# Optimization experiments

Hardware: AMD Instinct MI355X
Metric: run time of the kernel (lower is better)

## Reference

```python
import jax, jax.numpy as jnp
import numpy as np

N, IN_F, E, EDGE_F, H, C = 50000, 128, 800000, 32, 4, 32
NEG_SLOPE = 0.2
EPS = 1e-16


def setup_inputs() -> dict:
    key = jax.random.key(0)
    ks = jax.random.split(key, 10)
    s = lambda *sh: 1.0 / np.sqrt(sh[-1])
    return {
        "node_features": jax.random.normal(ks[0], (N, IN_F), jnp.float32),
        "edge_features": jax.random.normal(ks[1], (E, EDGE_F), jnp.float32),
        "edge_index": jax.random.randint(ks[2], (2, E), 0, N, jnp.int32),
        # GATConv params
        "W_gat": jax.random.normal(ks[3], (H * C, IN_F), jnp.float32) * s(IN_F),
        "att_src": jax.random.normal(ks[4], (H, C), jnp.float32) * s(C),
        "att_dst": jax.random.normal(ks[5], (H, C), jnp.float32) * s(C),
        "att_edge": jax.random.normal(ks[6], (H, C), jnp.float32) * s(C),
        "bias": jnp.zeros((H * C,), jnp.float32),
        # edge_linear and skip_connection weights
        "W_edge": jax.random.normal(ks[7], (H * C, EDGE_F), jnp.float32) * s(EDGE_F),
        "W_skip": jax.random.normal(ks[8], (H * C, IN_F), jnp.float32) * s(IN_F),
    }


def reference(node_features, edge_features, edge_index, W_gat, att_src, att_dst,
              att_edge, bias, W_edge, W_skip):
    src, dst = edge_index[0], edge_index[1]
    # edge_linear + view(-1, H, C)
    e_attr = (edge_features @ W_edge.T).reshape(E, H, C)
    # GATConv: per-head linear transform of nodes -> [N, H, C]
    x = (node_features @ W_gat.T).reshape(N, H, C)
    # attention logits: a_src.x_i + a_dst.x_j + a_edge.e  -> [E, H]
    a_src = jnp.einsum('nhc,hc->nh', x, att_src)
    a_dst = jnp.einsum('nhc,hc->nh', x, att_dst)
    a_edge = jnp.einsum('ehc,hc->eh', e_attr, att_edge)
    alpha = jax.nn.leaky_relu(a_src[src] + a_dst[dst] + a_edge, NEG_SLOPE)
    # segment softmax over incoming edges of each destination node
    m = jax.ops.segment_max(alpha, dst, num_segments=N)  # [N, H]
    m = jnp.where(jnp.isfinite(m), m, 0.0)
    ex = jnp.exp(alpha - m[dst])
    denom = jax.ops.segment_sum(ex, dst, num_segments=N)  # [N, H]
    attn = ex / (denom[dst] + EPS)  # [E, H]
    # message = alpha * x_src ; scatter-add to destination
    msg = x[src] * attn[:, :, None]  # [E, H, C]
    out = jax.ops.segment_sum(msg, dst, num_segments=N)  # [N, H, C]
    out = out.reshape(N, H * C) + bias  # concat=True
    # skip connection + ELU activation
    out = out + node_features @ W_skip.T
    return jax.nn.elu(out)
```

## Files before the change

kernel.cpp:

```cpp
#include <hip/hip_runtime.h>
#include <hip/hip_bf16.h>

constexpr int N_NODES = 50000;
constexpr int IN_F    = 128;
constexpr long E_EDGES = 800000;
constexpr int EDGE_F  = 32;
constexpr int H_HEADS = 4;
constexpr int C_CH    = 32;
constexpr int HC      = 128;
constexpr float NEG_SLOPE = 0.2f;
constexpr float EPS = 1e-16f;
constexpr int B_HIST = 64;
constexpr int B_WCAT = 8;
constexpr int CHUNK  = (int)(E_EDGES / B_HIST);
constexpr int HW8    = N_NODES / 4;
constexpr int NB_SCAN = (N_NODES + 255) / 256;
constexpr int NB_A    = (N_NODES + 3) / 4;
constexpr int NB_EL4  = (int)((E_EDGES + 1023) / 1024);
constexpr int NB_AE10 = (int)((E_EDGES + 511) / 512);
constexpr float SM_SHIFT = 12.0f;

typedef __attribute__((ext_vector_type(8))) short bf16x8;
typedef __attribute__((ext_vector_type(4))) float f32x4;

__device__ __forceinline__ unsigned short f2b(float f) {
    __hip_bfloat16 h = __float2bfloat16(f);
    return *reinterpret_cast<unsigned short*>(&h);
}
__device__ __forceinline__ float b2f_lo(unsigned v) { return __uint_as_float(v << 16); }
__device__ __forceinline__ float b2f_hi(unsigned v) { return __uint_as_float(v & 0xffff0000u); }

__global__ __launch_bounds__(1024) void mega1_kernel(
    const int* __restrict__ dst, unsigned int* __restrict__ histB,
    unsigned short* __restrict__ rank16, const float* __restrict__ ef,
    const float* __restrict__ We, const float* __restrict__ att_edge,
    const float* __restrict__ Wg, const float* __restrict__ Ws,
    unsigned short* __restrict__ wcat, float* __restrict__ ae)
{
    __shared__ unsigned int h[HW8];
    __shared__ float wf_lds[128];
    const int b = blockIdx.x, t = threadIdx.x;

    if (b < B_HIST) {
        for (int i = t; i < HW8; i += 1024) h[i] = 0;
        __syncthreads();
        const int e0 = b * CHUNK;
        for (int i = t; i < CHUNK; i += 1024) {
            int d = dst[e0 + i];
            int sh = (d & 3) * 8;
            unsigned old = atomicAdd(&h[d >> 2], 1u << sh);
            rank16[e0 + i] = (unsigned short)((old >> sh) & 0xFFu);
        }
        __syncthreads();
        unsigned int* outp = histB + (size_t)b * HW8;
        for (int i = t; i < HW8; i += 1024) outp[i] = h[i];
        return;
    }

    if (b < B_HIST + B_WCAT) {
        int i = ((b - B_HIST) * 1024 + t) * 4;
        const float* srcp = (i < 16384) ? (Wg + i) : (Ws + i - 16384);
        float4 v = *(const float4*)srcp;
        ushort4 o;
        o.x = f2b(v.x); o.y = f2b(v.y); o.z = f2b(v.z); o.w = f2b(v.w);
        *(ushort4*)&wcat[i] = o;
        return;
    }

    if (t < 128) {
        int hh = t >> 5, f = t & 31;
        float acc = 0.f;
#pragma unroll
        for (int c = 0; c < C_CH; ++c)
            acc = fmaf(We[(hh * C_CH + c) * EDGE_F + f], att_edge[hh * C_CH + c], acc);
        wf_lds[t] = acc;
    }
    __syncthreads();

    const int l = t & 63, wv = t >> 6;
    const int sub = l & 3, eIdx = l >> 2;
    const long eb = (long)(b - B_HIST - B_WCAT) * 512 + wv * 32 + eIdx;
    const float4* ef4 = (const float4*)ef;
    float4 wa[4], wb[4];
#pragma unroll
    for (int hh = 0; hh < 4; ++hh) {
        wa[hh] = *(const float4*)&wf_lds[hh * 32 + sub * 4];
        wb[hh] = *(const float4*)&wf_lds[hh * 32 + 16 + sub * 4];
    }

    if (eb < E_EDGES) {
        float4 a0 = ef4[eb * 8 + sub];
        float4 b0 = ef4[eb * 8 + 4 + sub];
        float p[4];
#pragma unroll
        for (int hh = 0; hh < 4; ++hh) {
            float acc = 0.f;
            acc = fmaf(a0.x, wa[hh].x, acc); acc = fmaf(a0.y, wa[hh].y, acc);
            acc = fmaf(a0.z, wa[hh].z, acc); acc = fmaf(a0.w, wa[hh].w, acc);
            acc = fmaf(b0.x, wb[hh].x, acc); acc = fmaf(b0.y, wb[hh].y, acc);
            acc = fmaf(b0.z, wb[hh].z, acc); acc = fmaf(b0.w, wb[hh].w, acc);
            p[hh] = acc;
        }
#pragma unroll
        for (int hh = 0; hh < 4; ++hh) {
            p[hh] += __shfl_xor(p[hh], 1);
            p[hh] += __shfl_xor(p[hh], 2);
        }
        float v0 = (sub == 0) ? p[0] : (sub == 1) ? p[1] : (sub == 2) ? p[2] : p[3];
        ae[eb * 4 + sub] = v0;
    }
    if (eb + 16 < E_EDGES) {
        float4 a1 = ef4[(eb + 16) * 8 + sub];
        float4 b1 = ef4[(eb + 16) * 8 + 4 + sub];
        float p[4];
#pragma unroll
        for (int hh = 0; hh < 4; ++hh) {
            float acc = 0.f;
            acc = fmaf(a1.x, wa[hh].x, acc); acc = fmaf(a1.y, wa[hh].y, acc);
            acc = fmaf(a1.z, wa[hh].z, acc); acc = fmaf(a1.w, wa[hh].w, acc);
            acc = fmaf(b1.x, wb[hh].x, acc); acc = fmaf(b1.y, wb[hh].y, acc);
            acc = fmaf(b1.z, wb[hh].z, acc); acc = fmaf(b1.w, wb[hh].w, acc);
            p[hh] = acc;
        }
#pragma unroll
        for (int hh = 0; hh < 4; ++hh) {
            p[hh] += __shfl_xor(p[hh], 1);
            p[hh] += __shfl_xor(p[hh], 2);
        }
        float v1 = (sub == 0) ? p[0] : (sub == 1) ? p[1] : (sub == 2) ? p[2] : p[3];
        ae[(eb + 16) * 4 + sub] = v1;
    }
}

__global__ __launch_bounds__(256) void mfma_gemm_kernel(
    const float* __restrict__ nf, const unsigned short* __restrict__ wcat,
    const float* __restrict__ bias, unsigned short* __restrict__ xb,
    float* __restrict__ out)
{
    const int t  = threadIdx.x;
    const int w  = t >> 6;
    const int l  = t & 63;
    const int lr = l & 15;
    const int lk = l >> 4;
    const int n0 = blockIdx.x * 64;

    bf16x8 bfr[4][4];
#pragma unroll
    for (int nfr = 0; nfr < 4; ++nfr)
#pragma unroll
        for (int ks = 0; ks < 4; ++ks)
            bfr[nfr][ks] = *(const bf16x8*)&wcat[(w * 64 + nfr * 16 + lr) * 128 + ks * 32 + lk * 8];

    f32x4 acc[4][4];
#pragma unroll
    for (int mf = 0; mf < 4; ++mf)
#pragma unroll
        for (int nfr = 0; nfr < 4; ++nfr)
            acc[mf][nfr] = (f32x4){0.f, 0.f, 0.f, 0.f};

#pragma unroll
    for (int ks = 0; ks < 4; ++ks) {
        bf16x8 afr[4];
#pragma unroll
        for (int mf = 0; mf < 4; ++mf) {
            int row = n0 + mf * 16 + lr;
            row = row < N_NODES ? row : N_NODES - 1;
            const float* ap = nf + (size_t)row * IN_F + ks * 32 + lk * 8;
            float4 a0 = *(const float4*)ap;
            float4 a1 = *(const float4*)(ap + 4);
            bf16x8 f;
            f[0] = (short)f2b(a0.x); f[1] = (short)f2b(a0.y);
            f[2] = (short)f2b(a0.z); f[3] = (short)f2b(a0.w);
            f[4] = (short)f2b(a1.x); f[5] = (short)f2b(a1.y);
            f[6] = (short)f2b(a1.z); f[7] = (short)f2b(a1.w);
            afr[mf] = f;
        }
#pragma unroll
        for (int mf = 0; mf < 4; ++mf)
#pragma unroll
            for (int nfr = 0; nfr < 4; ++nfr)
                acc[mf][nfr] = __builtin_amdgcn_mfma_f32_16x16x32_bf16(
                    afr[mf], bfr[nfr][ks], acc[mf][nfr], 0, 0, 0);
    }

#pragma unroll
    for (int nfr = 0; nfr < 4; ++nfr) {
        const int gc = w * 64 + nfr * 16 + lr;
        if (gc < HC) {
#pragma unroll
            for (int mf = 0; mf < 4; ++mf)
#pragma unroll
                for (int r = 0; r < 4; ++r) {
                    int m = n0 + mf * 16 + lk * 4 + r;
                    if (m < N_NODES) xb[(size_t)m * HC + gc] = f2b(acc[mf][nfr][r]);
                }
        } else {
            const float bv = bias[gc - HC];
#pragma unroll
            for (int mf = 0; mf < 4; ++mf)
#pragma unroll
                for (int r = 0; r < 4; ++r) {
                    int m = n0 + mf * 16 + lk * 4 + r;
                    if (m < N_NODES) out[(size_t)m * HC + gc - HC] = acc[mf][nfr][r] + bv;
                }
        }
    }
}

__global__ __launch_bounds__(256) void scan1_a_kernel(
    const unsigned int* __restrict__ histB, int* __restrict__ row_ptr,
    int* __restrict__ blocksum, const unsigned int* __restrict__ xb32,
    const float* __restrict__ att_src, const float* __restrict__ att_dst,
    float* __restrict__ asrc, float* __restrict__ adst)
{
    const int b = blockIdx.x, t = threadIdx.x;
    if (b < NB_SCAN) {
        __shared__ int s[256];
        int i = b * 256 + t;
        int v = 0;
        if (i < N_NODES) {
            int w = i >> 2, sh = (i & 3) * 8;
#pragma unroll 8
            for (int bb = 0; bb < B_HIST; ++bb)
                v += (int)((histB[(size_t)bb * HW8 + w] >> sh) & 0xFFu);
        }
        s[t] = v;
        __syncthreads();
#pragma unroll
        for (int off = 1; off < 256; off <<= 1) {
            int u = (t >= off) ? s[t - off] : 0;
            __syncthreads();
            s[t] += u;
            __syncthreads();
        }
        if (i < N_NODES) row_ptr[i] = s[t] - v;
        if (t == 255) blocksum[b] = s[255];
        return;
    }

    const int wave = t >> 6, lane = t & 63;
    const int n = (b - NB_SCAN) * 4 + wave;
    if (n >= N_NODES) return;
    unsigned v = xb32[(size_t)n * 64 + lane];
    float x0 = b2f_lo(v), x1 = b2f_hi(v);
    float2 as = ((const float2*)att_src)[lane];
    float2 ad = ((const float2*)att_dst)[lane];
    float ps = x0 * as.x + x1 * as.y;
    float pd = x0 * ad.x + x1 * ad.y;
#pragma unroll
    for (int off = 1; off < 16; off <<= 1) {
        ps += __shfl_xor(ps, off);
        pd += __shfl_xor(pd, off);
    }
    if ((lane & 15) == 0) {
        asrc[(size_t)n * H_HEADS + (lane >> 4)] = ps;
        adst[(size_t)n * H_HEADS + (lane >> 4)] = pd;
    }
}

__global__ __launch_bounds__(256) void scanF_kernel(int* __restrict__ row_ptr,
                                                    const int* __restrict__ blocksum,
                                                    const unsigned int* __restrict__ histB,
                                                    int* __restrict__ off)
{
    __shared__ int s[256];
    int t = threadIdx.x;
    int v = (t < NB_SCAN) ? blocksum[t] : 0;
    s[t] = v;
    __syncthreads();
#pragma unroll
    for (int o = 1; o < 256; o <<= 1) {
        int u = (t >= o) ? s[t - o] : 0;
        __syncthreads();
        s[t] += u;
        __syncthreads();
    }
    int excl = s[t] - v;
    __syncthreads();
    s[t] = excl;
    __syncthreads();
    const int blockoff = s[blockIdx.x];

    int i = blockIdx.x * 256 + t;
    if (i < N_NODES) {
        int run = row_ptr[i] + blockoff;
        row_ptr[i] = run;
        int w = i >> 2, sh = (i & 3) * 8;
#pragma unroll 8
        for (int b = 0; b < B_HIST; ++b) {
            off[(size_t)b * N_NODES + i] = run;
            run += (int)((histB[(size_t)b * HW8 + w] >> sh) & 0xFFu);
        }
    }
    if (i == 0) row_ptr[N_NODES] = (int)E_EDGES;
}

__global__ __launch_bounds__(256) void edge_logits_kernel(
    const int* __restrict__ src, const int* __restrict__ dst,
    const float* __restrict__ ae, const float* __restrict__ asrc,
    const float* __restrict__ adst, const int* __restrict__ off,
    const unsigned short* __restrict__ rank16, uint4* __restrict__ rec4)
{
    const long base = (long)blockIdx.x * 1024 + threadIdx.x;

    int s[4], d[4], rk[4];
    float4 a_e[4];
    bool val[4];
    long ec[4];
#pragma unroll
    for (int j = 0; j < 4; ++j) {
        long e = base + j * 256;
        val[j] = e < E_EDGES;
        ec[j] = val[j] ? e : 0;
        s[j]  = src[ec[j]];
        d[j]  = dst[ec[j]];
        rk[j] = (int)rank16[ec[j]];
        a_e[j] = ((const float4*)ae)[ec[j]];
    }
    float4 as4[4], ad4[4];
    int pos[4];
#pragma unroll
    for (int j = 0; j < 4; ++j) {
        as4[j] = ((const float4*)asrc)[s[j]];
        ad4[j] = ((const float4*)adst)[d[j]];
        int be = (int)(ec[j] / CHUNK);
        pos[j] = off[(size_t)be * N_NODES + d[j]] + rk[j];
    }
#pragma unroll
    for (int j = 0; j < 4; ++j) {
        if (!val[j]) continue;
        float lg[4] = {as4[j].x + ad4[j].x + a_e[j].x, as4[j].y + ad4[j].y + a_e[j].y,
                       as4[j].z + ad4[j].z + a_e[j].z, as4[j].w + ad4[j].w + a_e[j].w};
        uint4 r;
        unsigned* rw = (unsigned*)&r;
#pragma unroll
        for (int h = 0; h < 4; ++h) {
            float al = lg[h] > 0.f ? lg[h] : NEG_SLOPE * lg[h];
            rw[h] = (__float_as_uint(al) & 0xFFFFFF00u)
                  | ((unsigned)(s[j] >> (8 * h)) & 0xFFu);
        }
        rec4[pos[j]] = r;
    }
}

__device__ __forceinline__ void accum8(float* acc, uint4 v, float e) {
    acc[0] = fmaf(b2f_lo(v.x), e, acc[0]);
    acc[1] = fmaf(b2f_hi(v.x), e, acc[1]);
    acc[2] = fmaf(b2f_lo(v.y), e, acc[2]);
    acc[3] = fmaf(b2f_hi(v.y), e, acc[3]);
    acc[4] = fmaf(b2f_lo(v.z), e, acc[4]);
    acc[5] = fmaf(b2f_hi(v.z), e, acc[5]);
    acc[6] = fmaf(b2f_lo(v.w), e, acc[6]);
    acc[7] = fmaf(b2f_hi(v.w), e, acc[7]);
}

__device__ __forceinline__ int rec_src(uint4 r) {
    return (int)((r.x & 0xFFu) | ((r.y & 0xFFu) << 8));
}
__device__ __forceinline__ float rec_alpha(uint4 r, int h) {
    unsigned w = h == 0 ? r.x : h == 1 ? r.y : h == 2 ? r.z : r.w;
    return __uint_as_float(w & 0xFFFFFF00u);
}

__global__ __launch_bounds__(256) void aggregate_kernel(
    const int* __restrict__ row_ptr, const uint4* __restrict__ rec4,
    const uint4* __restrict__ xb4, float* __restrict__ out)
{
    const int wave = threadIdx.x >> 6;
    const int lane = threadIdx.x & 63;
    const int d = blockIdx.x * 4 + wave;
    if (d >= N_NODES) return;
    const int beg = row_ptr[d], end = row_ptr[d + 1];
    const int q  = lane >> 4;
    const int cg = lane & 15;
    const int h  = cg >> 2;

    float acc[8] = {0.f, 0.f, 0.f, 0.f, 0.f, 0.f, 0.f, 0.f};
    float dsum = 0.f;

    int i = beg;
    for (; i + 8 <= end; i += 8) {
        int i0 = i + q, i1 = i + 4 + q;
        uint4 r0 = rec4[i0];
        uint4 r1 = rec4[i1];
        int s0 = rec_src(r0);
        int s1 = rec_src(r1);
        float a0 = rec_alpha(r0, h);
        float a1 = rec_alpha(r1, h);
        uint4 v0 = xb4[(size_t)s0 * 16 + cg];
        uint4 v1 = xb4[(size_t)s1 * 16 + cg];
        float e0 = __expf(a0 - SM_SHIFT);
        float e1 = __expf(a1 - SM_SHIFT);
        dsum += e0 + e1;
        accum8(acc, v0, e0);
        accum8(acc, v1, e1);
    }
    for (; i < end; i += 4) {
        int idx = i + q;
        bool val = idx < end;
        int ii = val ? idx : end - 1;
        uint4 r = rec4[ii];
        int s = rec_src(r);
        float a = rec_alpha(r, h);
        uint4 v = xb4[(size_t)s * 16 + cg];
        float e = val ? __expf(a - SM_SHIFT) : 0.f;
        dsum += e;
        accum8(acc, v, e);
    }

#pragma unroll
    for (int off = 16; off <= 32; off <<= 1) {
        dsum += __shfl_xor(dsum, off);
#pragma unroll
        for (int k = 0; k < 8; ++k) acc[k] += __shfl_xor(acc[k], off);
    }
    const float inv = 1.f / (dsum + EPS);

    if (q == 0) {
        float* op = out + (size_t)d * HC + cg * 8;
        float4 o0 = *(const float4*)op;
        float4 o1 = *(const float4*)(op + 4);
        o0.x += acc[0] * inv; o0.y += acc[1] * inv;
        o0.z += acc[2] * inv; o0.w += acc[3] * inv;
        o1.x += acc[4] * inv; o1.y += acc[5] * inv;
        o1.z += acc[6] * inv; o1.w += acc[7] * inv;
        o0.x = o0.x > 0.f ? o0.x : expf(o0.x) - 1.f;
        o0.y = o0.y > 0.f ? o0.y : expf(o0.y) - 1.f;
        o0.z = o0.z > 0.f ? o0.z : expf(o0.z) - 1.f;
        o0.w = o0.w > 0.f ? o0.w : expf(o0.w) - 1.f;
        o1.x = o1.x > 0.f ? o1.x : expf(o1.x) - 1.f;
        o1.y = o1.y > 0.f ? o1.y : expf(o1.y) - 1.f;
        o1.z = o1.z > 0.f ? o1.z : expf(o1.z) - 1.f;
        o1.w = o1.w > 0.f ? o1.w : expf(o1.w) - 1.f;
        *(float4*)op = o0;
        *(float4*)(op + 4) = o1;
    }
}

extern "C" void kernel_launch(void* const* d_in, const int* in_sizes, int n_in,
                              void* d_out, int out_size, void* d_ws, size_t ws_size,
                              hipStream_t stream)
{
    const float* nf       = (const float*)d_in[0];
    const float* ef       = (const float*)d_in[1];
    const int*   ei       = (const int*)d_in[2];
    const float* Wg       = (const float*)d_in[3];
    const float* att_src  = (const float*)d_in[4];
    const float* att_dst  = (const float*)d_in[5];
    const float* att_edge = (const float*)d_in[6];
    const float* bias     = (const float*)d_in[7];
    const float* We       = (const float*)d_in[8];
    const float* Ws       = (const float*)d_in[9];
    float* out = (float*)d_out;

    const int* src = ei;
    const int* dst = ei + E_EDGES;

    unsigned int* rec   = (unsigned int*)d_ws;
    float* ae           = (float*)(rec + 4 * E_EDGES);
    unsigned short* xb  = (unsigned short*)(ae + 4 * E_EDGES);
    unsigned short* wcat= xb + (size_t)N_NODES * HC;
    float* asrc         = (float*)(wcat + 256 * 128);
    float* adst         = asrc + (size_t)N_NODES * H_HEADS;
    unsigned int* histB = (unsigned int*)(adst + (size_t)N_NODES * H_HEADS);
    int*   off          = (int*)(histB + (size_t)B_HIST * HW8);
    int*   row_ptr      = off + (size_t)B_HIST * N_NODES;
    int*   blocksum     = row_ptr + N_NODES + 1;
    unsigned short* rank16 = (unsigned short*)(blocksum + 256);

    mega1_kernel<<<B_HIST + B_WCAT + NB_AE10, 1024, 0, stream>>>(
        dst, histB, rank16, ef, We, att_edge, Wg, Ws, wcat, ae);
    mfma_gemm_kernel<<<(N_NODES + 63) / 64, 256, 0, stream>>>(
        nf, wcat, bias, xb, out);
    scan1_a_kernel<<<NB_SCAN + NB_A, 256, 0, stream>>>(
        histB, row_ptr, blocksum, (const unsigned int*)xb,
        att_src, att_dst, asrc, adst);
    scanF_kernel<<<NB_SCAN, 256, 0, stream>>>(row_ptr, blocksum, histB, off);
    edge_logits_kernel<<<NB_EL4, 256, 0, stream>>>(
        src, dst, ae, asrc, adst, off, rank16, (uint4*)rec);
    aggregate_kernel<<<(N_NODES + 3) / 4, 256, 0, stream>>>(
        row_ptr, (const uint4*)rec, (const uint4*)xb, out);
}
```

Before: 155.6 us.

## Fuse node GEMM into the histogram/edge-projection megakernel, converting weights inline

Removes the separate weight-conversion blocks and the standalone MFMA GEMM launch. The node-feature GEMM now runs as extra 1024-thread blocks inside the first megakernel, four 64-row tiles per block, and each wave reads the fp32 Wg/Ws weights and converts them to bf16 on the fly. This saves one kernel launch and its dependency barrier, and lets the GEMM overlap with the histogram and edge-logit work. In exchange every wave re-reads and re-converts the weights, and 1024-thread blocks holding 16 accumulator fragments per wave may cut occupancy.

```diff
diff --git a/kernel.cpp b/kernel.cpp
--- a/kernel.cpp
+++ b/kernel.cpp
@@ -11,7 +11,8 @@
 constexpr float NEG_SLOPE = 0.2f;
 constexpr float EPS = 1e-16f;
 constexpr int B_HIST = 64;
-constexpr int B_WCAT = 8;
+constexpr int NT_GEMM = (N_NODES + 63) / 64;
+constexpr int NB_GEMM = (NT_GEMM + 3) / 4;
 constexpr int CHUNK  = (int)(E_EDGES / B_HIST);
 constexpr int HW8    = N_NODES / 4;
 constexpr int NB_SCAN = (N_NODES + 255) / 256;
@@ -30,12 +31,25 @@
 __device__ __forceinline__ float b2f_lo(unsigned v) { return __uint_as_float(v << 16); }
 __device__ __forceinline__ float b2f_hi(unsigned v) { return __uint_as_float(v & 0xffff0000u); }
 
-__global__ __launch_bounds__(1024) void mega1_kernel(
+__device__ __forceinline__ bf16x8 cvt8(const float* p) {
+    float4 a = *(const float4*)p;
+    float4 b = *(const float4*)(p + 4);
+    bf16x8 f;
+    f[0] = (short)f2b(a.x); f[1] = (short)f2b(a.y);
+    f[2] = (short)f2b(a.z); f[3] = (short)f2b(a.w);
+    f[4] = (short)f2b(b.x); f[5] = (short)f2b(b.y);
+    f[6] = (short)f2b(b.z); f[7] = (short)f2b(b.w);
+    return f;
+}
+
+__global__ __launch_bounds__(1024) void mega_kernel(
     const int* __restrict__ dst, unsigned int* __restrict__ histB,
     unsigned short* __restrict__ rank16, const float* __restrict__ ef,
     const float* __restrict__ We, const float* __restrict__ att_edge,
     const float* __restrict__ Wg, const float* __restrict__ Ws,
-    unsigned short* __restrict__ wcat, float* __restrict__ ae)
+    float* __restrict__ ae, const float* __restrict__ nf,
+    const float* __restrict__ bias, unsigned short* __restrict__ xb,
+    float* __restrict__ out)
 {
     __shared__ unsigned int h[HW8];
     __shared__ float wf_lds[128];
@@ -57,13 +71,71 @@
         return;
     }
 
-    if (b < B_HIST + B_WCAT) {
-        int i = ((b - B_HIST) * 1024 + t) * 4;
-        const float* srcp = (i < 16384) ? (Wg + i) : (Ws + i - 16384);
-        float4 v = *(const float4*)srcp;
-        ushort4 o;
-        o.x = f2b(v.x); o.y = f2b(v.y); o.z = f2b(v.z); o.w = f2b(v.w);
-        *(ushort4*)&wcat[i] = o;
+    if (b < B_HIST + NB_GEMM) {
+        const int w16 = t >> 6;
+        const int l  = t & 63;
+        const int lr = l & 15;
+        const int lk = l >> 4;
+        const int tile = (b - B_HIST) * 4 + (w16 >> 2);
+        if (tile >= NT_GEMM) return;
+        const int wc = w16 & 3;
+        const int n0 = tile * 64;
+
+        f32x4 acc[4][4];
+#pragma unroll
+        for (int mf = 0; mf < 4; ++mf)
+#pragma unroll
+            for (int nfr = 0; nfr < 4; ++nfr)
+                acc[mf][nfr] = (f32x4){0.f, 0.f, 0.f, 0.f};
+
+#pragma unroll
+        for (int ks = 0; ks < 4; ++ks) {
+            bf16x8 bfr[4];
+#pragma unroll
+            for (int nfr = 0; nfr < 4; ++nfr) {
+                int gr = wc * 64 + nfr * 16 + lr;
+                const float* wp = (gr < HC ? Wg + (size_t)gr * IN_F
+                                           : Ws + (size_t)(gr - HC) * IN_F)
+                                  + ks * 32 + lk * 8;
+                bfr[nfr] = cvt8(wp);
+            }
+            bf16x8 afr[4];
+#pragma unroll
+            for (int mf = 0; mf < 4; ++mf) {
+                int row = n0 + mf * 16 + lr;
+                row = row < N_NODES ? row : N_NODES - 1;
+                afr[mf] = cvt8(nf + (size_t)row * IN_F + ks * 32 + lk * 8);
+            }
+#pragma unroll
+            for (int mf = 0; mf < 4; ++mf)
+#pragma unroll
+                for (int nfr = 0; nfr < 4; ++nfr)
+                    acc[mf][nfr] = __builtin_amdgcn_mfma_f32_16x16x32_bf16(
+                        afr[mf], bfr[nfr], acc[mf][nfr], 0, 0, 0);
+        }
+
+#pragma unroll
+        for (int nfr = 0; nfr < 4; ++nfr) {
+            const int gc = wc * 64 + nfr * 16 + lr;
+            if (gc < HC) {
+#pragma unroll
+                for (int mf = 0; mf < 4; ++mf)
+#pragma unroll
+                    for (int r = 0; r < 4; ++r) {
+                        int m = n0 + mf * 16 + lk * 4 + r;
+                        if (m < N_NODES) xb[(size_t)m * HC + gc] = f2b(acc[mf][nfr][r]);
+                    }
+            } else {
+                const float bv = bias[gc - HC];
+#pragma unroll
+                for (int mf = 0; mf < 4; ++mf)
+#pragma unroll
+                    for (int r = 0; r < 4; ++r) {
+                        int m = n0 + mf * 16 + lk * 4 + r;
+                        if (m < N_NODES) out[(size_t)m * HC + gc - HC] = acc[mf][nfr][r] + bv;
+                    }
+            }
+        }
         return;
     }
 
@@ -79,7 +151,7 @@
 
     const int l = t & 63, wv = t >> 6;
     const int sub = l & 3, eIdx = l >> 2;
-    const long eb = (long)(b - B_HIST - B_WCAT) * 512 + wv * 32 + eIdx;
+    const long eb = (long)(b - B_HIST - NB_GEMM) * 512 + wv * 32 + eIdx;
     const float4* ef4 = (const float4*)ef;
     float4 wa[4], wb[4];
 #pragma unroll
@@ -129,81 +201,6 @@
         }
         float v1 = (sub == 0) ? p[0] : (sub == 1) ? p[1] : (sub == 2) ? p[2] : p[3];
         ae[(eb + 16) * 4 + sub] = v1;
-    }
-}
-
-__global__ __launch_bounds__(256) void mfma_gemm_kernel(
-    const float* __restrict__ nf, const unsigned short* __restrict__ wcat,
-    const float* __restrict__ bias, unsigned short* __restrict__ xb,
-    float* __restrict__ out)
-{
-    const int t  = threadIdx.x;
-    const int w  = t >> 6;
-    const int l  = t & 63;
-    const int lr = l & 15;
-    const int lk = l >> 4;
-    const int n0 = blockIdx.x * 64;
-
-    bf16x8 bfr[4][4];
-#pragma unroll
-    for (int nfr = 0; nfr < 4; ++nfr)
-#pragma unroll
-        for (int ks = 0; ks < 4; ++ks)
-            bfr[nfr][ks] = *(const bf16x8*)&wcat[(w * 64 + nfr * 16 + lr) * 128 + ks * 32 + lk * 8];
-
-    f32x4 acc[4][4];
-#pragma unroll
-    for (int mf = 0; mf < 4; ++mf)
-#pragma unroll
-        for (int nfr = 0; nfr < 4; ++nfr)
-            acc[mf][nfr] = (f32x4){0.f, 0.f, 0.f, 0.f};
-
-#pragma unroll
-    for (int ks = 0; ks < 4; ++ks) {
-        bf16x8 afr[4];
-#pragma unroll
-        for (int mf = 0; mf < 4; ++mf) {
-            int row = n0 + mf * 16 + lr;
-            row = row < N_NODES ? row : N_NODES - 1;
-            const float* ap = nf + (size_t)row * IN_F + ks * 32 + lk * 8;
-            float4 a0 = *(const float4*)ap;
-            float4 a1 = *(const float4*)(ap + 4);
-            bf16x8 f;
-            f[0] = (short)f2b(a0.x); f[1] = (short)f2b(a0.y);
-            f[2] = (short)f2b(a0.z); f[3] = (short)f2b(a0.w);
-            f[4] = (short)f2b(a1.x); f[5] = (short)f2b(a1.y);
-            f[6] = (short)f2b(a1.z); f[7] = (short)f2b(a1.w);
-            afr[mf] = f;
-        }
-#pragma unroll
-        for (int mf = 0; mf < 4; ++mf)
-#pragma unroll
-            for (int nfr = 0; nfr < 4; ++nfr)
-                acc[mf][nfr] = __builtin_amdgcn_mfma_f32_16x16x32_bf16(
-                    afr[mf], bfr[nfr][ks], acc[mf][nfr], 0, 0, 0);
-    }
-
-#pragma unroll
-    for (int nfr = 0; nfr < 4; ++nfr) {
-        const int gc = w * 64 + nfr * 16 + lr;
-        if (gc < HC) {
-#pragma unroll
-            for (int mf = 0; mf < 4; ++mf)
-#pragma unroll
-                for (int r = 0; r < 4; ++r) {
-                    int m = n0 + mf * 16 + lk * 4 + r;
-                    if (m < N_NODES) xb[(size_t)m * HC + gc] = f2b(acc[mf][nfr][r]);
-                }
-        } else {
-            const float bv = bias[gc - HC];
-#pragma unroll
-            for (int mf = 0; mf < 4; ++mf)
-#pragma unroll
-                for (int r = 0; r < 4; ++r) {
-                    int m = n0 + mf * 16 + lk * 4 + r;
-                    if (m < N_NODES) out[(size_t)m * HC + gc - HC] = acc[mf][nfr][r] + bv;
-                }
-        }
     }
 }
 
@@ -459,8 +456,7 @@
     unsigned int* rec   = (unsigned int*)d_ws;
     float* ae           = (float*)(rec + 4 * E_EDGES);
     unsigned short* xb  = (unsigned short*)(ae + 4 * E_EDGES);
-    unsigned short* wcat= xb + (size_t)N_NODES * HC;
-    float* asrc         = (float*)(wcat + 256 * 128);
+    float* asrc         = (float*)(xb + (size_t)N_NODES * HC);
     float* adst         = asrc + (size_t)N_NODES * H_HEADS;
     unsigned int* histB = (unsigned int*)(adst + (size_t)N_NODES * H_HEADS);
     int*   off          = (int*)(histB + (size_t)B_HIST * HW8);
@@ -468,10 +464,8 @@
     int*   blocksum     = row_ptr + N_NODES + 1;
     unsigned short* rank16 = (unsigned short*)(blocksum + 256);
 
-    mega1_kernel<<<B_HIST + B_WCAT + NB_AE10, 1024, 0, stream>>>(
-        dst, histB, rank16, ef, We, att_edge, Wg, Ws, wcat, ae);
-    mfma_gemm_kernel<<<(N_NODES + 63) / 64, 256, 0, stream>>>(
-        nf, wcat, bias, xb, out);
+    mega_kernel<<<B_HIST + NB_GEMM + NB_AE10, 1024, 0, stream>>>(
+        dst, histB, rank16, ef, We, att_edge, Wg, Ws, ae, nf, bias, xb, out);
     scan1_a_kernel<<<NB_SCAN + NB_A, 256, 0, stream>>>(
         histB, row_ptr, blocksum, (const unsigned int*)xb,
         att_src, att_dst, asrc, adst);
```

Result: faster. 144.9 us (-6.9%).
